# Performance work log

Measured on AMD Instinct MI355X. Metric: run time of the kernel, lower is better.

The kernel has to match this reference:

```python
import jax, jax.numpy as jnp
import numpy as np

N_NODES = 50000
N_EDGES = 1600000
D_IN = 128
D_HID = 128
D_OUT = 128


def setup_inputs() -> dict:
    key = jax.random.key(0)
    k1, k2, k3, k4, k5, k6 = jax.random.split(key, 6)
    x = jax.random.normal(k1, (N_NODES, D_IN), dtype=jnp.float32)
    edge_index = jax.random.randint(k2, (2, N_EDGES), 0, N_NODES, dtype=jnp.int64)
    # glorot-ish init for GCNConv linear weights; bias zeros-like but randomized small
    W1 = jax.random.normal(k3, (D_IN, D_HID), dtype=jnp.float32) * (1.0 / np.sqrt(D_IN))
    b1 = jax.random.normal(k4, (D_HID,), dtype=jnp.float32) * 0.01
    W2 = jax.random.normal(k5, (D_HID, D_OUT), dtype=jnp.float32) * (1.0 / np.sqrt(D_HID))
    b2 = jax.random.normal(k6, (D_OUT,), dtype=jnp.float32) * 0.01
    return {"x": x, "edge_index": edge_index, "W1": W1, "b1": b1, "W2": W2, "b2": b2}


def gcn_conv(x, src, dst, W, b, n_nodes):
    # PyG GCNConv: add self-loops, symmetric normalization deg^-1/2, lin -> aggregate -> +bias
    loop = jnp.arange(n_nodes, dtype=src.dtype)
    s = jnp.concatenate([src, loop])  # [E+N]
    d = jnp.concatenate([dst, loop])  # [E+N]
    deg = jax.ops.segment_sum(jnp.ones_like(d, dtype=x.dtype), d, num_segments=n_nodes)
    dinv = jnp.where(deg > 0, jax.lax.rsqrt(deg), 0.0)
    norm = dinv[s] * dinv[d]  # [E+N]
    h = x @ W  # [N, F_out]
    msg = h[s] * norm[:, None]  # gather + scale: [E+N, F_out]
    out = jax.ops.segment_sum(msg, d, num_segments=n_nodes)  # scatter-add
    return out + b


def reference(x, edge_index, W1, b1, W2, b2):
    src, dst = edge_index[0], edge_index[1]
    h = gcn_conv(x, src, dst, W1, b1, N_NODES)
    h = jnp.where(h >= 0, h, 0.1 * h)  # LeakyReLU(0.1)
    h = gcn_conv(h, src, dst, W2, b2, N_NODES)
    return h.mean(axis=1)  # [N]
```

## Files before the change

kernel.cpp:

```cpp
#include <hip/hip_runtime.h>
#include <hip/hip_bf16.h>


#define N_NODES 50000
#define NPAD 50048
#define D 128
#define BK 196
#define CHUNK 4096

typedef unsigned int uint;
typedef unsigned short u16;

__device__ __forceinline__ uint pack_bf2(float a, float b) {
    uint ua = __float_as_uint(a), ub = __float_as_uint(b);
    ua = (ua + 0x7fffu + ((ua >> 16) & 1u)) >> 16;
    ub = (ub + 0x7fffu + ((ub >> 16) & 1u)) >> 16;
    return ua | (ub << 16);
}

__global__ void hist_kernel(const int* __restrict__ dst, uint* __restrict__ H, int E, int CHN) {
    __shared__ uint h[BK];
    int t = threadIdx.x, c = blockIdx.x;
    if (t < BK) h[t] = 0;
    __syncthreads();
    int e0 = c * CHUNK;
    for (int i = t; i < CHUNK; i += 256) {
        int e = e0 + i;
        if (e < E) atomicAdd(&h[dst[e] >> 8], 1u);
    }
    __syncthreads();
    if (t < BK) H[t * CHN + c] = h[t];
}

__global__ void colscan_kernel(uint* __restrict__ H, uint* __restrict__ T, int CHN) {
    __shared__ uint s[256];
    int t = threadIdx.x, b = blockIdx.x;
    uint carry = 0;
    for (int base = 0; base < CHN; base += 256) {
        int idx = base + t;
        uint v = (idx < CHN) ? H[b * CHN + idx] : 0u;
        s[t] = v;
        __syncthreads();
#pragma unroll
        for (int off = 1; off < 256; off <<= 1) {
            uint u = (t >= off) ? s[t - off] : 0u;
            __syncthreads();
            s[t] += u;
            __syncthreads();
        }
        if (idx < CHN) H[b * CHN + idx] = carry + s[t] - v;
        carry += s[255];
        __syncthreads();
    }
    if (t == 0) T[b] = carry;
}

__global__ void totscan_kernel(const uint* __restrict__ T, uint* __restrict__ B,
                               int* __restrict__ row, int E, int N) {
    __shared__ uint s[256];
    int t = threadIdx.x;
    uint v = (t < BK) ? T[t] : 0u;
    s[t] = v;
    __syncthreads();
#pragma unroll
    for (int off = 1; off < 256; off <<= 1) {
        uint u = (t >= off) ? s[t - off] : 0u;
        __syncthreads();
        s[t] += u;
        __syncthreads();
    }
    if (t < BK) B[t] = s[t] - v;
    if (t == 0) { B[BK] = (uint)E; row[N] = E; }
}

__global__ void scatter_kernel(const int* __restrict__ src, const int* __restrict__ dst,
                               const uint* __restrict__ H, const uint* __restrict__ B,
                               uint* __restrict__ EB, int E, int CHN) {
    __shared__ uint cur[BK];
    int t = threadIdx.x, c = blockIdx.x;
    if (t < BK) cur[t] = B[t] + H[t * CHN + c];
    __syncthreads();
    int e0 = c * CHUNK;
    for (int i = t; i < CHUNK; i += 256) {
        int e = e0 + i;
        if (e < E) {
            int d = dst[e];
            uint slot = atomicAdd(&cur[d >> 8], 1u);
            EB[slot] = ((uint)(d & 255) << 16) | (uint)src[e];
        }
    }
}

__global__ void bucket_sort_kernel(const uint* __restrict__ EB, const uint* __restrict__ B,
                                   int* __restrict__ row, float* __restrict__ dinv,
                                   u16* __restrict__ esrc, int N) {
    __shared__ uint cnt[256], s[256], cur[256];
    int t = threadIdx.x, b = blockIdx.x;
    uint base = B[b], ne = B[b + 1] - base;
    cnt[t] = 0;
    __syncthreads();
    for (uint i = t; i < ne; i += 256) atomicAdd(&cnt[EB[base + i] >> 16], 1u);
    __syncthreads();
    uint c = cnt[t];
    s[t] = c;
    __syncthreads();
#pragma unroll
    for (int off = 1; off < 256; off <<= 1) {
        uint u = (t >= off) ? s[t - off] : 0u;
        __syncthreads();
        s[t] += u;
        __syncthreads();
    }
    uint p = s[t] - c;
    int v = (b << 8) + t;
    if (v < N) {
        row[v] = (int)(base + p);
        dinv[v] = rsqrtf((float)(c + 1u));
    }
    cur[t] = base + p;
    __syncthreads();
    for (uint i = t; i < ne; i += 256) {
        uint u = EB[base + i];
        uint slot = atomicAdd(&cur[u >> 16], 1u);
        esrc[slot] = (u16)(u & 0xffffu);
    }
}

__global__ void w2m_kernel(const float* __restrict__ W2, const float* __restrict__ b2,
                           float* __restrict__ w2m) {
    int k = blockIdx.x, lane = threadIdx.x;
    const float* p = (k < 128) ? (W2 + k * 128) : b2;
    float s = p[lane] + p[lane + 64];
#pragma unroll
    for (int off = 32; off > 0; off >>= 1) s += __shfl_down(s, off, 64);
    if (lane == 0) w2m[k] = s * (1.0f / 128.0f);
}

#define TM 64
__global__ __launch_bounds__(256) void gemm_kernel(
    const float* __restrict__ A, const float* __restrict__ W,
    uint* __restrict__ G16, const float* __restrict__ dinv, int M) {
    __shared__ float Ws[64 * 128];
    __shared__ float As[TM * 128];
    int t = threadIdx.x;
    int row0 = blockIdx.x * TM;

    {
        float4* Asv = (float4*)As;
#pragma unroll
        for (int i = 0; i < (TM * 32) / 256; i++) {
            int f = t + i * 256;
            int r = f >> 5;
            int c4 = f & 31;
            int row = row0 + r;
            float4 v = make_float4(0.f, 0.f, 0.f, 0.f);
            if (row < M) v = ((const float4*)(A + (long)row * D))[c4];
            Asv[f] = v;
        }
    }

    int tx = t & 31;
    int ty = t >> 5;
    float4 acc[8];
#pragma unroll
    for (int r = 0; r < 8; r++) acc[r] = make_float4(0.f, 0.f, 0.f, 0.f);

    const float4* Wsv = (const float4*)Ws;
    for (int ph = 0; ph < 2; ph++) {
        __syncthreads();
        {
            const float4* Wv = (const float4*)(W + ph * 64 * 128);
            float4* Wsv_w = (float4*)Ws;
#pragma unroll
            for (int i = 0; i < 8; i++) Wsv_w[t + i * 256] = Wv[t + i * 256];
        }
        __syncthreads();
        for (int k = 0; k < 64; k += 4) {
            float4 w0 = Wsv[(k + 0) * 32 + tx];
            float4 w1 = Wsv[(k + 1) * 32 + tx];
            float4 w2 = Wsv[(k + 2) * 32 + tx];
            float4 w3 = Wsv[(k + 3) * 32 + tx];
#pragma unroll
            for (int r = 0; r < 8; r++) {
                int row = ty * 8 + r;
                float4 a = *(const float4*)(As + row * 128 + ph * 64 + k);
                acc[r].x += a.x * w0.x + a.y * w1.x + a.z * w2.x + a.w * w3.x;
                acc[r].y += a.x * w0.y + a.y * w1.y + a.z * w2.y + a.w * w3.y;
                acc[r].z += a.x * w0.z + a.y * w1.z + a.z * w2.z + a.w * w3.z;
                acc[r].w += a.x * w0.w + a.y * w1.w + a.z * w2.w + a.w * w3.w;
            }
        }
    }
#pragma unroll
    for (int r = 0; r < 8; r++) {
        int row = row0 + ty * 8 + r;
        if (row < M) {
            float dv = dinv[row];
            uint2 o;
            o.x = pack_bf2(acc[r].x * dv, acc[r].y * dv);
            o.y = pack_bf2(acc[r].z * dv, acc[r].w * dv);
            ((uint2*)G16)[(long)row * 32 + tx] = o;
        }
    }
}

__global__ __launch_bounds__(256) void gather_node_kernel(
    const int* __restrict__ row, const u16* __restrict__ esrc,
    const uint* __restrict__ g16, const float* __restrict__ dinv,
    const float* __restrict__ b1, const float* __restrict__ w2m,
    float* __restrict__ mg, int N) {
    int wave = threadIdx.x >> 6;
    int lane = threadIdx.x & 63;
    int sub = lane & 15;
    int grp = lane >> 4;
    int v = blockIdx.x * 4 + wave;
    if (v >= N) return;

    const uint4* gv = (const uint4*)g16;
    float a0 = 0.f, a1 = 0.f, a2 = 0.f, a3 = 0.f, a4 = 0.f, a5 = 0.f, a6 = 0.f, a7 = 0.f;

#define ACCUM(u)                                                        \
    a0 += __uint_as_float((u).x << 16); a1 += __uint_as_float((u).x & 0xffff0000u); \
    a2 += __uint_as_float((u).y << 16); a3 += __uint_as_float((u).y & 0xffff0000u); \
    a4 += __uint_as_float((u).z << 16); a5 += __uint_as_float((u).z & 0xffff0000u); \
    a6 += __uint_as_float((u).w << 16); a7 += __uint_as_float((u).w & 0xffff0000u);

    if (grp == 0) {
        uint4 u = gv[(long)v * 16 + sub];
        ACCUM(u)
    }
    int jb = row[v], je = row[v + 1];
    int j = jb + grp;
    for (; j + 4 < je; j += 8) {
        int s0 = esrc[j], s1 = esrc[j + 4];
        uint4 u0 = gv[(long)s0 * 16 + sub];
        uint4 u1 = gv[(long)s1 * 16 + sub];
        ACCUM(u0)
        ACCUM(u1)
    }
    for (; j < je; j += 4) {
        int s = esrc[j];
        uint4 u = gv[(long)s * 16 + sub];
        ACCUM(u)
    }
#undef ACCUM

#define RED(a) a += __shfl_xor(a, 16, 64); a += __shfl_xor(a, 32, 64);
    RED(a0) RED(a1) RED(a2) RED(a3) RED(a4) RED(a5) RED(a6) RED(a7)
#undef RED

    if (grp == 0) {
        float dv = dinv[v];
        const float2* bp = (const float2*)b1;
        const float2* wp = (const float2*)w2m;
        float s = 0.f;
        float2 bb, wm;
        bb = bp[4 * sub + 0]; wm = wp[4 * sub + 0];
        float t0 = dv * a0 + bb.x; t0 = t0 >= 0.f ? t0 : 0.1f * t0;
        float t1 = dv * a1 + bb.y; t1 = t1 >= 0.f ? t1 : 0.1f * t1;
        s += t0 * wm.x + t1 * wm.y;
        bb = bp[4 * sub + 1]; wm = wp[4 * sub + 1];
        t0 = dv * a2 + bb.x; t0 = t0 >= 0.f ? t0 : 0.1f * t0;
        t1 = dv * a3 + bb.y; t1 = t1 >= 0.f ? t1 : 0.1f * t1;
        s += t0 * wm.x + t1 * wm.y;
        bb = bp[4 * sub + 2]; wm = wp[4 * sub + 2];
        t0 = dv * a4 + bb.x; t0 = t0 >= 0.f ? t0 : 0.1f * t0;
        t1 = dv * a5 + bb.y; t1 = t1 >= 0.f ? t1 : 0.1f * t1;
        s += t0 * wm.x + t1 * wm.y;
        bb = bp[4 * sub + 3]; wm = wp[4 * sub + 3];
        t0 = dv * a6 + bb.x; t0 = t0 >= 0.f ? t0 : 0.1f * t0;
        t1 = dv * a7 + bb.y; t1 = t1 >= 0.f ? t1 : 0.1f * t1;
        s += t0 * wm.x + t1 * wm.y;
        s += __shfl_xor(s, 1, 64);
        s += __shfl_xor(s, 2, 64);
        s += __shfl_xor(s, 4, 64);
        s += __shfl_xor(s, 8, 64);
        if (sub == 0) mg[v] = dv * s;
    }
}

__global__ void out_kernel(const int* __restrict__ row, const u16* __restrict__ esrc,
                           const float* __restrict__ mg, const float* __restrict__ dinv,
                           const float* __restrict__ w2m, float* __restrict__ out, int N) {
    int v = blockIdx.x * blockDim.x + threadIdx.x;
    if (v >= N) return;
    float acc = mg[v];
    int jb = row[v], je = row[v + 1];
    int j = jb;
    for (; j + 8 <= je; j += 8) {
        acc += mg[esrc[j]] + mg[esrc[j + 1]] + mg[esrc[j + 2]] + mg[esrc[j + 3]] +
               mg[esrc[j + 4]] + mg[esrc[j + 5]] + mg[esrc[j + 6]] + mg[esrc[j + 7]];
    }
    for (; j < je; j++) acc += mg[esrc[j]];
    out[v] = dinv[v] * acc + w2m[128];
}

extern "C" void kernel_launch(void* const* d_in, const int* in_sizes, int n_in,
                              void* d_out, int out_size, void* d_ws, size_t ws_size,
                              hipStream_t stream) {
    const float* x  = (const float*)d_in[0];
    const int* ei   = (const int*)d_in[1];
    const float* W1 = (const float*)d_in[2];
    const float* b1 = (const float*)d_in[3];
    const float* W2 = (const float*)d_in[4];
    const float* b2 = (const float*)d_in[5];
    float* out = (float*)d_out;

    const int N = N_NODES;
    const int E = in_sizes[1] / 2;
    const int* src = ei;
    const int* dst = ei + E;
    const int CHN = (E + CHUNK - 1) / CHUNK;
    const int nblocks = (N + 255) / 256;

    float*    dinv = (float*)d_ws;
    int*      row  = (int*)(dinv + NPAD);
    uint*     B    = (uint*)(row + NPAD + 16);
    float*    w2m  = (float*)(B + 256);
    float*    mg   = w2m + 256;
    uint*     T    = (uint*)(mg + NPAD);
    uint*     H    = T + 256;
    u16*      esrc = (u16*)(H + BK * CHN);
    uint*     g16  = (uint*)(esrc + E + (E & 1));
    uint*     EB   = g16;

    hist_kernel<<<CHN, 256, 0, stream>>>(dst, H, E, CHN);
    colscan_kernel<<<BK, 256, 0, stream>>>(H, T, CHN);
    totscan_kernel<<<1, 256, 0, stream>>>(T, B, row, E, N);
    scatter_kernel<<<CHN, 256, 0, stream>>>(src, dst, H, B, EB, E, CHN);
    bucket_sort_kernel<<<BK, 256, 0, stream>>>(EB, B, row, dinv, esrc, N);

    w2m_kernel<<<129, 64, 0, stream>>>(W2, b2, w2m);

    gemm_kernel<<<(N + TM - 1) / TM, 256, 0, stream>>>(x, W1, g16, dinv, N);

    gather_node_kernel<<<(N + 3) / 4, 256, 0, stream>>>(row, esrc, g16, dinv, b1, w2m, mg, N);

    out_kernel<<<nblocks, 256, 0, stream>>>(row, esrc, mg, dinv, w2m, out, N);
}
```

Before: 239.4 us.

## Use bf16 MFMA for feature GEMM and restructure gather with 8-lane rows

Replaces the fp32 FMA tiled GEMM with a bf16 MFMA 16x16x32 kernel. W is transposed into padded LDS and A fragments are converted to bf16 in registers, which cuts the GEMM's ALU cost but adds rounding of inputs to bf16. The gather kernel now uses 8 lanes per row, each loading 32 bytes, so 8 neighbors are handled per wave, and it software-prefetches the next neighbor row. The workspace layout is also rearranged so the g16 buffer sits before esrc and H.

```diff
diff --git a/kernel.cpp b/kernel.cpp
--- a/kernel.cpp
+++ b/kernel.cpp
@@ -10,12 +10,15 @@
 
 typedef unsigned int uint;
 typedef unsigned short u16;
-
+typedef __attribute__((ext_vector_type(8))) short short8;
+typedef __attribute__((ext_vector_type(4))) float floatx4;
+
+__device__ __forceinline__ u16 cvt_bf16(float f) {
+    uint u = __float_as_uint(f);
+    return (u16)((u + 0x7fffu + ((u >> 16) & 1u)) >> 16);
+}
 __device__ __forceinline__ uint pack_bf2(float a, float b) {
-    uint ua = __float_as_uint(a), ub = __float_as_uint(b);
-    ua = (ua + 0x7fffu + ((ua >> 16) & 1u)) >> 16;
-    ub = (ub + 0x7fffu + ((ub >> 16) & 1u)) >> 16;
-    return ua | (ub << 16);
+    return (uint)cvt_bf16(a) | ((uint)cvt_bf16(b) << 16);
 }
 
 __global__ void hist_kernel(const int* __restrict__ dst, uint* __restrict__ H, int E, int CHN) {
@@ -136,70 +139,63 @@
     if (lane == 0) w2m[k] = s * (1.0f / 128.0f);
 }
 
-#define TM 64
-__global__ __launch_bounds__(256) void gemm_kernel(
+#define WT_STRIDE 136
+__global__ __launch_bounds__(256) void gemm_mfma_kernel(
     const float* __restrict__ A, const float* __restrict__ W,
-    uint* __restrict__ G16, const float* __restrict__ dinv, int M) {
-    __shared__ float Ws[64 * 128];
-    __shared__ float As[TM * 128];
+    u16* __restrict__ G16, const float* __restrict__ dinv, int M) {
+    __shared__ u16 Wt[128 * WT_STRIDE];
     int t = threadIdx.x;
-    int row0 = blockIdx.x * TM;
-
-    {
-        float4* Asv = (float4*)As;
-#pragma unroll
-        for (int i = 0; i < (TM * 32) / 256; i++) {
-            int f = t + i * 256;
-            int r = f >> 5;
-            int c4 = f & 31;
-            int row = row0 + r;
-            float4 v = make_float4(0.f, 0.f, 0.f, 0.f);
-            if (row < M) v = ((const float4*)(A + (long)row * D))[c4];
-            Asv[f] = v;
-        }
-    }
-
-    int tx = t & 31;
-    int ty = t >> 5;
-    float4 acc[8];
-#pragma unroll
-    for (int r = 0; r < 8; r++) acc[r] = make_float4(0.f, 0.f, 0.f, 0.f);
-
-    const float4* Wsv = (const float4*)Ws;
-    for (int ph = 0; ph < 2; ph++) {
-        __syncthreads();
-        {
-            const float4* Wv = (const float4*)(W + ph * 64 * 128);
-            float4* Wsv_w = (float4*)Ws;
-#pragma unroll
-            for (int i = 0; i < 8; i++) Wsv_w[t + i * 256] = Wv[t + i * 256];
-        }
-        __syncthreads();
-        for (int k = 0; k < 64; k += 4) {
-            float4 w0 = Wsv[(k + 0) * 32 + tx];
-            float4 w1 = Wsv[(k + 1) * 32 + tx];
-            float4 w2 = Wsv[(k + 2) * 32 + tx];
-            float4 w3 = Wsv[(k + 3) * 32 + tx];
-#pragma unroll
-            for (int r = 0; r < 8; r++) {
-                int row = ty * 8 + r;
-                float4 a = *(const float4*)(As + row * 128 + ph * 64 + k);
-                acc[r].x += a.x * w0.x + a.y * w1.x + a.z * w2.x + a.w * w3.x;
-                acc[r].y += a.x * w0.y + a.y * w1.y + a.z * w2.y + a.w * w3.y;
-                acc[r].z += a.x * w0.z + a.y * w1.z + a.z * w2.z + a.w * w3.z;
-                acc[r].w += a.x * w0.w + a.y * w1.w + a.z * w2.w + a.w * w3.w;
+    for (int i = t; i < 128 * 128; i += 256) {
+        int k = i >> 7, n = i & 127;
+        Wt[n * WT_STRIDE + k] = cvt_bf16(W[i]);
+    }
+    __syncthreads();
+
+    int wave = t >> 6, lane = t & 63;
+    int m = lane & 15, quad = lane >> 4;
+    int rowa = blockIdx.x * 64 + wave * 16 + m;
+    int rowc = rowa < M ? rowa : M - 1;
+    const float* Arow = A + (long)rowc * D;
+
+    short8 afrag[4];
+#pragma unroll
+    for (int kt = 0; kt < 4; kt++) {
+        int k0 = kt * 32 + quad * 8;
+        float4 f0 = *(const float4*)(Arow + k0);
+        float4 f1 = *(const float4*)(Arow + k0 + 4);
+        short8 af;
+        af[0] = (short)cvt_bf16(f0.x); af[1] = (short)cvt_bf16(f0.y);
+        af[2] = (short)cvt_bf16(f0.z); af[3] = (short)cvt_bf16(f0.w);
+        af[4] = (short)cvt_bf16(f1.x); af[5] = (short)cvt_bf16(f1.y);
+        af[6] = (short)cvt_bf16(f1.z); af[7] = (short)cvt_bf16(f1.w);
+        afrag[kt] = af;
+    }
+
+    int orow0 = blockIdx.x * 64 + wave * 16;
+    float dv[4]; bool ok[4];
+#pragma unroll
+    for (int r = 0; r < 4; r++) {
+        int orow = orow0 + quad * 4 + r;
+        ok[r] = orow < M;
+        dv[r] = dinv[ok[r] ? orow : (M - 1)];
+    }
+
+    uint* G32 = (uint*)G16;
+    for (int n0 = 0; n0 < 128; n0 += 16) {
+        floatx4 acc = {0.f, 0.f, 0.f, 0.f};
+#pragma unroll
+        for (int kt = 0; kt < 4; kt++) {
+            short8 bf = *(const short8*)(Wt + (n0 + m) * WT_STRIDE + kt * 32 + quad * 8);
+            acc = __builtin_amdgcn_mfma_f32_16x16x32_bf16(afrag[kt], bf, acc, 0, 0, 0);
+        }
+#pragma unroll
+        for (int r = 0; r < 4; r++) {
+            float val = acc[r] * dv[r];
+            float oth = __shfl_xor(val, 1, 64);
+            if (ok[r] && (m & 1) == 0) {
+                int orow = orow0 + quad * 4 + r;
+                G32[(long)orow * 64 + ((n0 + m) >> 1)] = pack_bf2(val, oth);
             }
-        }
-    }
-#pragma unroll
-    for (int r = 0; r < 8; r++) {
-        int row = row0 + ty * 8 + r;
-        if (row < M) {
-            float dv = dinv[row];
-            uint2 o;
-            o.x = pack_bf2(acc[r].x * dv, acc[r].y * dv);
-            o.y = pack_bf2(acc[r].z * dv, acc[r].w * dv);
-            ((uint2*)G16)[(long)row * 32 + tx] = o;
         }
     }
 }
@@ -211,71 +207,72 @@
     float* __restrict__ mg, int N) {
     int wave = threadIdx.x >> 6;
     int lane = threadIdx.x & 63;
-    int sub = lane & 15;
-    int grp = lane >> 4;
+    int sub = lane & 7;
+    int nb = lane >> 3;
     int v = blockIdx.x * 4 + wave;
     if (v >= N) return;
 
     const uint4* gv = (const uint4*)g16;
-    float a0 = 0.f, a1 = 0.f, a2 = 0.f, a3 = 0.f, a4 = 0.f, a5 = 0.f, a6 = 0.f, a7 = 0.f;
-
-#define ACCUM(u)                                                        \
-    a0 += __uint_as_float((u).x << 16); a1 += __uint_as_float((u).x & 0xffff0000u); \
-    a2 += __uint_as_float((u).y << 16); a3 += __uint_as_float((u).y & 0xffff0000u); \
-    a4 += __uint_as_float((u).z << 16); a5 += __uint_as_float((u).z & 0xffff0000u); \
-    a6 += __uint_as_float((u).w << 16); a7 += __uint_as_float((u).w & 0xffff0000u);
-
-    if (grp == 0) {
-        uint4 u = gv[(long)v * 16 + sub];
-        ACCUM(u)
+    float acc[16];
+#pragma unroll
+    for (int i = 0; i < 16; i++) acc[i] = 0.f;
+
+#define ACC8(ua, ub) {                                                   \
+    uint uu[8] = {(ua).x, (ua).y, (ua).z, (ua).w, (ub).x, (ub).y, (ub).z, (ub).w}; \
+    _Pragma("unroll")                                                    \
+    for (int i = 0; i < 8; i++) {                                        \
+        acc[2*i]   += __uint_as_float(uu[i] << 16);                      \
+        acc[2*i+1] += __uint_as_float(uu[i] & 0xffff0000u);              \
+    } }
+
+    if (nb == 0) {
+        long rb = (long)v * 16 + 2 * sub;
+        uint4 ua = gv[rb], ub = gv[rb + 1];
+        ACC8(ua, ub)
     }
     int jb = row[v], je = row[v + 1];
-    int j = jb + grp;
-    for (; j + 4 < je; j += 8) {
-        int s0 = esrc[j], s1 = esrc[j + 4];
-        uint4 u0 = gv[(long)s0 * 16 + sub];
-        uint4 u1 = gv[(long)s1 * 16 + sub];
-        ACCUM(u0)
-        ACCUM(u1)
-    }
-    for (; j < je; j += 4) {
-        int s = esrc[j];
-        uint4 u = gv[(long)s * 16 + sub];
-        ACCUM(u)
-    }
-#undef ACCUM
-
-#define RED(a) a += __shfl_xor(a, 16, 64); a += __shfl_xor(a, 32, 64);
-    RED(a0) RED(a1) RED(a2) RED(a3) RED(a4) RED(a5) RED(a6) RED(a7)
-#undef RED
-
-    if (grp == 0) {
-        float dv = dinv[v];
-        const float2* bp = (const float2*)b1;
-        const float2* wp = (const float2*)w2m;
+    int j = jb + nb;
+    if (j < je) {
+        long r0 = (long)esrc[j] * 16 + 2 * sub;
+        uint4 p0 = gv[r0], p1 = gv[r0 + 1];
+        j += 8;
+        while (j < je) {
+            long r1 = (long)esrc[j] * 16 + 2 * sub;
+            uint4 q0 = gv[r1], q1 = gv[r1 + 1];
+            j += 8;
+            ACC8(p0, p1)
+            p0 = q0; p1 = q1;
+        }
+        ACC8(p0, p1)
+    }
+#undef ACC8
+
+#pragma unroll
+    for (int i = 0; i < 16; i++) {
+        acc[i] += __shfl_xor(acc[i], 8, 64);
+        acc[i] += __shfl_xor(acc[i], 16, 64);
+        acc[i] += __shfl_xor(acc[i], 32, 64);
+    }
+
+    if (nb == 0) {
+        float dvv = dinv[v];
+        const float4* bp = (const float4*)b1;
+        const float4* wp = (const float4*)w2m;
         float s = 0.f;
-        float2 bb, wm;
-        bb = bp[4 * sub + 0]; wm = wp[4 * sub + 0];
-        float t0 = dv * a0 + bb.x; t0 = t0 >= 0.f ? t0 : 0.1f * t0;
-        float t1 = dv * a1 + bb.y; t1 = t1 >= 0.f ? t1 : 0.1f * t1;
-        s += t0 * wm.x + t1 * wm.y;
-        bb = bp[4 * sub + 1]; wm = wp[4 * sub + 1];
-        t0 = dv * a2 + bb.x; t0 = t0 >= 0.f ? t0 : 0.1f * t0;
-        t1 = dv * a3 + bb.y; t1 = t1 >= 0.f ? t1 : 0.1f * t1;
-        s += t0 * wm.x + t1 * wm.y;
-        bb = bp[4 * sub + 2]; wm = wp[4 * sub + 2];
-        t0 = dv * a4 + bb.x; t0 = t0 >= 0.f ? t0 : 0.1f * t0;
-        t1 = dv * a5 + bb.y; t1 = t1 >= 0.f ? t1 : 0.1f * t1;
-        s += t0 * wm.x + t1 * wm.y;
-        bb = bp[4 * sub + 3]; wm = wp[4 * sub + 3];
-        t0 = dv * a6 + bb.x; t0 = t0 >= 0.f ? t0 : 0.1f * t0;
-        t1 = dv * a7 + bb.y; t1 = t1 >= 0.f ? t1 : 0.1f * t1;
-        s += t0 * wm.x + t1 * wm.y;
+#pragma unroll
+        for (int q4 = 0; q4 < 4; q4++) {
+            float4 bb = bp[sub * 4 + q4];
+            float4 wm = wp[sub * 4 + q4];
+            float t0 = dvv * acc[4*q4 + 0] + bb.x; t0 = t0 >= 0.f ? t0 : 0.1f * t0;
+            float t1 = dvv * acc[4*q4 + 1] + bb.y; t1 = t1 >= 0.f ? t1 : 0.1f * t1;
+            float t2 = dvv * acc[4*q4 + 2] + bb.z; t2 = t2 >= 0.f ? t2 : 0.1f * t2;
+            float t3 = dvv * acc[4*q4 + 3] + bb.w; t3 = t3 >= 0.f ? t3 : 0.1f * t3;
+            s += t0 * wm.x + t1 * wm.y + t2 * wm.z + t3 * wm.w;
+        }
         s += __shfl_xor(s, 1, 64);
         s += __shfl_xor(s, 2, 64);
         s += __shfl_xor(s, 4, 64);
-        s += __shfl_xor(s, 8, 64);
-        if (sub == 0) mg[v] = dv * s;
+        if (sub == 0) mg[v] = dvv * s;
     }
 }
 
@@ -319,10 +316,10 @@
     float*    w2m  = (float*)(B + 256);
     float*    mg   = w2m + 256;
     uint*     T    = (uint*)(mg + NPAD);
-    uint*     H    = T + 256;
-    u16*      esrc = (u16*)(H + BK * CHN);
-    uint*     g16  = (uint*)(esrc + E + (E & 1));
-    uint*     EB   = g16;
+    uint*     g16u = T + 256;
+    u16*      esrc = (u16*)(g16u + NPAD * 64);
+    uint*     H    = (uint*)(esrc + E + (E & 1));
+    uint*     EB   = g16u;
 
     hist_kernel<<<CHN, 256, 0, stream>>>(dst, H, E, CHN);
     colscan_kernel<<<BK, 256, 0, stream>>>(H, T, CHN);
@@ -332,9 +329,9 @@
 
     w2m_kernel<<<129, 64, 0, stream>>>(W2, b2, w2m);
 
-    gemm_kernel<<<(N + TM - 1) / TM, 256, 0, stream>>>(x, W1, g16, dinv, N);
-
-    gather_node_kernel<<<(N + 3) / 4, 256, 0, stream>>>(row, esrc, g16, dinv, b1, w2m, mg, N);
+    gemm_mfma_kernel<<<(N + 63) / 64, 256, 0, stream>>>(x, W1, (u16*)g16u, dinv, N);
+
+    gather_node_kernel<<<(N + 3) / 4, 256, 0, stream>>>(row, esrc, g16u, dinv, b1, w2m, mg, N);
 
     out_kernel<<<nblocks, 256, 0, stream>>>(row, esrc, mg, dinv, w2m, out, N);
 }
```

After: 217.1 us. -9.3%, faster.
